# Optimization experiments

Hardware: AMD Instinct MI355X
Metric: run time of the kernel (lower is better)

The kernel has to match this reference:

```python
import jax, jax.numpy as jnp
import numpy as np

IMG_SIZE = 512
NUM_FREQ_MASKS = 4


def _make_masks(n, num):
    # Mirrors DCTTransform._generate_freq_masks: for i in reversed(range(num-1)),
    # an anti-triangular (low-frequency) mask of size n//2**i padded to (n,n),
    # then an all-ones mask appended last.
    masks = []
    for i in reversed(range(num - 1)):
        m = n // (2 ** i)
        tri = np.triu(np.ones((m, m), dtype=np.float32))      # upper triangular
        rot = np.rot90(tri, k=1)                               # -> i+j <= m-1 region
        pad = np.zeros((n, n), dtype=np.float32)
        pad[:m, :m] = rot
        masks.append(pad)
    masks.append(np.ones((n, n), dtype=np.float32))
    return np.stack(masks)  # [num, n, n]


def _dct_matrix(n, dtype=jnp.float32):
    # Orthonormal DCT-II matrix: X = D @ x  ==  scipy.fftpack.dct(x, axis=0, norm='ortho')
    k = jnp.arange(n, dtype=dtype)[:, None]
    m = jnp.arange(n, dtype=dtype)[None, :]
    D = jnp.cos(jnp.pi * (2.0 * m + 1.0) * k / (2.0 * n)) * jnp.sqrt(2.0 / n)
    D = D.at[0].multiply(1.0 / jnp.sqrt(2.0))  # k=0 row scale -> sqrt(1/n)
    return D


def setup_inputs() -> dict:
    key = jax.random.key(0)
    x = jax.random.normal(key, (32, 3, IMG_SIZE, IMG_SIZE), dtype=jnp.float32)
    masks = jnp.asarray(_make_masks(IMG_SIZE, NUM_FREQ_MASKS))
    return {"x": x, "masks": masks}


def reference(x, masks):
    # x: [B, C, H, W] with H == W == img_size; masks: [4, H, W]
    n = x.shape[-1]
    D = _dct_matrix(n, x.dtype)
    # 2D orthonormal DCT-II over last two axes: D @ x @ D^T (separable, order-free)
    dct2 = jnp.einsum('ij,bcjk,lk->bcil', D, x, D)
    outs = []
    for i in range(masks.shape[0]):  # small fixed loop over 4 masks
        masked = dct2 * masks[i]
        # inverse 2D DCT (IDCT-II == DCT-III, orthonormal): D^T @ y @ D
        outs.append(jnp.einsum('ji,bcjk,kl->bcil', D, masked, D))
    LH, HL, HH, LL = outs  # idx 0->LH, 1->HL, 2->HH, 3(ones)->LL per original forward
    return (LL, LH, HL, HH)
```

## Files before the change

### kernel.cpp

```cpp
#include <hip/hip_runtime.h>
#include <hip/hip_bf16.h>
#include <stdint.h>

#define NIMG 96
#define N 512
#define IMG (N*N)
#define OUT_PLANE ((long long)NIMG * IMG)

typedef __attribute__((ext_vector_type(8))) _Float16 f16x8;
typedef __attribute__((ext_vector_type(4))) float f32x4;
typedef unsigned short u16;

__device__ inline u16 f2h(float v) {
    _Float16 h = (_Float16)v;
    return __builtin_bit_cast(u16, h);
}

__device__ inline void gload16(const void* g, void* l) {
    __builtin_amdgcn_global_load_lds(
        (const __attribute__((address_space(1))) void*)g,
        (__attribute__((address_space(3))) void*)l, 16, 0, 0);
}

__global__ void build_D(u16* __restrict__ Drm, u16* __restrict__ Dcm) {
    int idx = blockIdx.x * 256 + threadIdx.x;
    int k = idx >> 9, m = idx & 511;
    int r = ((2 * m + 1) * k) & 2047;
    float c = cospif((float)r * (1.0f / 1024.0f));
    float s = (k == 0) ? 0.04419417382415922f : 0.0625f;
    u16 h = f2h(c * s);
    Drm[k * 512 + m] = h;
    Dcm[m * 512 + k] = h;
}

__global__ __launch_bounds__(256) void conv_x(const float* __restrict__ x,
                                              u16* __restrict__ Xcm) {
    __shared__ float t[32][33];
    const long long base = (long long)blockIdx.z * IMG;
    const int r0 = blockIdx.y * 32, c0 = blockIdx.x * 32;
    const int tr = threadIdx.x >> 3;
    const int tc = (threadIdx.x & 7) * 4;
    float4 v = *(const float4*)&x[base + (long long)(r0 + tr) * N + c0 + tc];
    t[tr][tc + 0] = v.x; t[tr][tc + 1] = v.y;
    t[tr][tc + 2] = v.z; t[tr][tc + 3] = v.w;
    __syncthreads();
    ushort4 h;
    h.x = f2h(t[tc + 0][tr]); h.y = f2h(t[tc + 1][tr]);
    h.z = f2h(t[tc + 2][tr]); h.w = f2h(t[tc + 3][tr]);
    *(ushort4*)&Xcm[base + (long long)(c0 + tr) * N + r0 + tc] = h;
}

__global__ __launch_bounds__(256) void maskcopy(const u16* __restrict__ Y,
                                                u16* __restrict__ Z,
                                                int W, int lim) {
    long long idx = (long long)blockIdx.x * 256 + threadIdx.x;
    int wq = W >> 2;
    long long perimg = (long long)W * wq;
    int img = (int)(idx / perimg);
    long long rem = idx % perimg;
    int j = (int)(rem / wq);
    int i = (int)(rem % wq) * 4;
    ushort4 v = *(const ushort4*)&Y[(long long)img * IMG + (long long)j * N + i];
    if (i + 0 + j > lim) v.x = 0;
    if (i + 1 + j > lim) v.y = 0;
    if (i + 2 + j > lim) v.z = 0;
    if (i + 3 + j > lim) v.w = 0;
    *(ushort4*)&Z[(long long)img * W * W + (long long)j * W + i] = v;
}

template<int EPI>
__global__ __launch_bounds__(256) void gemm16(
    const u16* __restrict__ A, long long sA, int lda,
    const u16* __restrict__ B, long long sB, int ldb,
    void* __restrict__ Cv, long long sC, int ldc,
    int K, int trilim)
{
    __shared__ u16 As[2][128 * 32];
    __shared__ u16 Bs[2][128 * 32];

    const int bz = blockIdx.z;
    const int m0 = blockIdx.y * 128;
    const int n0 = blockIdx.x * 128;
    const int tid = threadIdx.x;
    const int wave = tid >> 6;
    const int lane = tid & 63;

    const u16* __restrict__ Ab = A + (long long)bz * sA;
    const u16* __restrict__ Bb = B + (long long)bz * sB;

    const int srow = lane >> 2;
    const int sc8  = (lane & 3) * 8;
    const int war  = wave * 32;

    const int fr  = lane & 15;
    const int kg8 = (lane >> 4) * 8;
    const int wr  = (wave >> 1) * 64;
    const int wc  = (wave & 1) * 64;

    int aoff[4], boff[4];
    #pragma unroll
    for (int i = 0; i < 4; ++i) {
        aoff[i] = (wr + i * 16 + fr) * 32 + kg8;
        boff[i] = (wc + i * 16 + fr) * 32 + kg8;
    }

    f32x4 acc[4][4];
    #pragma unroll
    for (int i = 0; i < 4; ++i)
        #pragma unroll
        for (int j = 0; j < 4; ++j)
            acc[i][j] = (f32x4){0.0f, 0.0f, 0.0f, 0.0f};

    auto stage = [&](int buf, int k0) {
        #pragma unroll
        for (int i = 0; i < 2; ++i) {
            int r = war + i * 16;
            gload16(Ab + (long long)(m0 + r + srow) * lda + k0 + sc8, &As[buf][r * 32]);
            gload16(Bb + (long long)(n0 + r + srow) * ldb + k0 + sc8, &Bs[buf][r * 32]);
        }
    };
    auto compute = [&](int buf) {
        f16x8 af[4], bf[4];
        #pragma unroll
        for (int i = 0; i < 4; ++i) af[i] = *(const f16x8*)&As[buf][aoff[i]];
        #pragma unroll
        for (int j = 0; j < 4; ++j) bf[j] = *(const f16x8*)&Bs[buf][boff[j]];
        #pragma unroll
        for (int i = 0; i < 4; ++i)
            #pragma unroll
            for (int j = 0; j < 4; ++j)
                acc[i][j] = __builtin_amdgcn_mfma_f32_16x16x32_f16(af[i], bf[j], acc[i][j], 0, 0, 0);
    };

    const int nb = K >> 5;
    stage(0, 0);
    __syncthreads();
    int cur = 0;
    for (int t = 0; t < nb - 1; ++t) {
        stage(cur ^ 1, (t + 1) * 32);
        compute(cur);
        __syncthreads();
        cur ^= 1;
    }
    compute(cur);

    const int rb = (lane >> 4) * 4;
    if (EPI == 0) {
        float* Cb = (float*)Cv + (long long)bz * sC;
        #pragma unroll
        for (int i = 0; i < 4; ++i)
            #pragma unroll
            for (int j = 0; j < 4; ++j) {
                int r = m0 + wr + i * 16 + rb;
                int c = n0 + wc + j * 16 + fr;
                #pragma unroll
                for (int g = 0; g < 4; ++g)
                    Cb[(long long)(r + g) * ldc + c] = acc[i][j][g];
            }
    } else if (EPI == 1) {
        u16* Cb = (u16*)Cv + (long long)bz * sC;
        #pragma unroll
        for (int i = 0; i < 4; ++i)
            #pragma unroll
            for (int j = 0; j < 4; ++j) {
                int r = m0 + wr + i * 16 + rb;
                int c = n0 + wc + j * 16 + fr;
                #pragma unroll
                for (int g = 0; g < 4; ++g)
                    Cb[(long long)(r + g) * ldc + c] = f2h(acc[i][j][g]);
            }
    } else {
        u16* Cb = (u16*)Cv + (long long)bz * sC;
        #pragma unroll
        for (int i = 0; i < 4; ++i)
            #pragma unroll
            for (int j = 0; j < 4; ++j) {
                int r = m0 + wr + i * 16 + rb;
                int c = n0 + wc + j * 16 + fr;
                ushort4 h;
                float v0 = ((r + 0) + c <= trilim) ? acc[i][j][0] : 0.0f;
                float v1 = ((r + 1) + c <= trilim) ? acc[i][j][1] : 0.0f;
                float v2 = ((r + 2) + c <= trilim) ? acc[i][j][2] : 0.0f;
                float v3 = ((r + 3) + c <= trilim) ? acc[i][j][3] : 0.0f;
                h.x = f2h(v0); h.y = f2h(v1); h.z = f2h(v2); h.w = f2h(v3);
                *(ushort4*)&Cb[(long long)c * ldc + r] = h;
            }
    }
}

extern "C" void kernel_launch(void* const* d_in, const int* in_sizes, int n_in,
                              void* d_out, int out_size, void* d_ws, size_t ws_size,
                              hipStream_t stream) {
    const float* x = (const float*)d_in[0];
    float* out = (float*)d_out;
    float* outLL = out + 0 * OUT_PLANE;
    float* outLH = out + 1 * OUT_PLANE;
    float* outHL = out + 2 * OUT_PLANE;
    float* outHH = out + 3 * OUT_PLANE;

    char* ws = (char*)d_ws;
    u16* Drm = (u16*)(ws);
    u16* Dcm = (u16*)(ws + 524288);
    u16* Xcm = (u16*)(ws + 1048576);
    u16* Ycm = Xcm;
    char* reg = ws + 51380224;
    u16* T1 = (u16*)reg;
    u16* U  = (u16*)reg;
    u16* U2 = (u16*)reg;
    u16* U3 = (u16*)reg;
    u16* Y2 = (u16*)(reg + 25165824);
    u16* Y3 = (u16*)(reg + 37748736);

    const long long S = IMG;
    const int BIG = 1 << 30;

    build_D<<<dim3(IMG / 256), 256, 0, stream>>>(Drm, Dcm);
    conv_x<<<dim3(16, 16, NIMG), 256, 0, stream>>>(x, Xcm);

    gemm16<1><<<dim3(4, 4, NIMG), 256, 0, stream>>>(
        Drm, 0, 512, Xcm, S, 512, T1, S, 512, 512, 0);
    gemm16<2><<<dim3(4, 4, NIMG), 256, 0, stream>>>(
        T1, S, 512, Drm, 0, 512, Ycm, S, 512, 512, 511);
    gemm16<2><<<dim3(4, 4, NIMG), 256, 0, stream>>>(
        Ycm, S, 512, Dcm, 0, 512, U, S, 512, 512, BIG);
    gemm16<0><<<dim3(4, 4, NIMG), 256, 0, stream>>>(
        U, S, 512, Dcm, 0, 512, outHH, S, 512, 512, 0);

    maskcopy<<<dim3(NIMG * 256 * 256 / 4 / 256), 256, 0, stream>>>(Ycm, Y2, 256, 255);
    maskcopy<<<dim3(NIMG * 128 * 128 / 4 / 256), 256, 0, stream>>>(Ycm, Y3, 128, 127);

    gemm16<2><<<dim3(4, 2, NIMG), 256, 0, stream>>>(
        Y2, 256 * 256, 256, Dcm, 0, 512, U2, 512 * 256, 256, 256, BIG);
    gemm16<0><<<dim3(4, 4, NIMG), 256, 0, stream>>>(
        U2, 512 * 256, 256, Dcm, 0, 512, outHL, S, 512, 256, 0);

    gemm16<2><<<dim3(4, 1, NIMG), 256, 0, stream>>>(
        Y3, 128 * 128, 128, Dcm, 0, 512, U3, 512 * 128, 128, 128, BIG);
    gemm16<0><<<dim3(4, 4, NIMG), 256, 0, stream>>>(
        U3, 512 * 128, 128, Dcm, 0, 512, outLH, S, 512, 128, 0);

    hipMemcpyAsync(outLL, x, (size_t)OUT_PLANE * sizeof(float),
                   hipMemcpyDeviceToDevice, stream);
}
```

Before: 364.0 us.

## Restructure DCT GEMMs: full-K LDS staging, fused inverse launches, triangular skipping

Replaces the double-buffered 128x128 GEMM with a 256x64 tile kernel that stages the whole B panel into swizzled LDS once and streams A fragments straight from global memory. The three first-stage inverse GEMMs are fused into one launch (invA) that shortens K for the triangular-masked inputs, and the two low-band second-stage GEMMs are fused into invB. Tiles lying fully outside the triangular mask exit early. The LL copy is folded into the transpose kernel, and scratch buffers are moved into the HH output region. This adds LDS pressure and uncoalesced A loads from global memory, and depends on the HH output being written last.

Measured after the change: 481.1 us. 1.32x slower.

```diff
diff --git a/kernel.cpp b/kernel.cpp
--- a/kernel.cpp
+++ b/kernel.cpp
@@ -11,15 +11,9 @@
 typedef __attribute__((ext_vector_type(4))) float f32x4;
 typedef unsigned short u16;
 
-__device__ inline u16 f2h(float v) {
+__device__ __forceinline__ u16 f2h(float v) {
     _Float16 h = (_Float16)v;
     return __builtin_bit_cast(u16, h);
-}
-
-__device__ inline void gload16(const void* g, void* l) {
-    __builtin_amdgcn_global_load_lds(
-        (const __attribute__((address_space(1))) void*)g,
-        (__attribute__((address_space(3))) void*)l, 16, 0, 0);
 }
 
 __global__ void build_D(u16* __restrict__ Drm, u16* __restrict__ Dcm) {
@@ -34,13 +28,15 @@
 }
 
 __global__ __launch_bounds__(256) void conv_x(const float* __restrict__ x,
-                                              u16* __restrict__ Xcm) {
+                                              u16* __restrict__ Xcm,
+                                              float* __restrict__ outLL) {
     __shared__ float t[32][33];
     const long long base = (long long)blockIdx.z * IMG;
     const int r0 = blockIdx.y * 32, c0 = blockIdx.x * 32;
     const int tr = threadIdx.x >> 3;
     const int tc = (threadIdx.x & 7) * 4;
     float4 v = *(const float4*)&x[base + (long long)(r0 + tr) * N + c0 + tc];
+    *(float4*)&outLL[base + (long long)(r0 + tr) * N + c0 + tc] = v;
     t[tr][tc + 0] = v.x; t[tr][tc + 1] = v.y;
     t[tr][tc + 2] = v.z; t[tr][tc + 3] = v.w;
     __syncthreads();
@@ -68,91 +64,111 @@
     *(ushort4*)&Z[(long long)img * W * W + (long long)j * W + i] = v;
 }
 
+#define WAVE_DECLS                                                          \
+    const int wave = threadIdx.x >> 6;                                      \
+    const int lane = threadIdx.x & 63;                                      \
+    const int fr   = lane & 15;                                             \
+    const int kg8  = (lane >> 4) << 3;                                      \
+    const int rb   = (lane >> 4) << 2;
+
+#define GEMM_STAGE(Bp, ldb, Keff, lds, PITCHB)                              \
+    {                                                                       \
+        const int cpr = (Keff) >> 3;                \
+        const int csh = 31 - __builtin_clz(cpr);                            \
+        const int total = cpr << 6;                                        \
+        for (int c = threadIdx.x; c < total; c += 256) {                    \
+            int n  = c >> csh;                                              \
+            int kb = (c & (cpr - 1)) << 4;                                  \
+            f16x8 v = *(const f16x8*)((Bp) + (long long)n * (ldb) + (kb >> 1)); \
+            *(f16x8*)((u16*)(lds) + ((n * (PITCHB) + (kb ^ ((n & 7) << 4))) >> 1)) = v; \
+        }                                                                   \
+        __syncthreads();                                                    \
+    }
+
+#define GEMM_MAIN(Ab, lda, Keff, lds, PITCHB)                               \
+    f32x4 acc[4][4];                                                        \
+    _Pragma("unroll")                                                       \
+    for (int i = 0; i < 4; ++i)                                             \
+        _Pragma("unroll")                                                   \
+        for (int j = 0; j < 4; ++j)                                         \
+            acc[i][j] = (f32x4){0.0f, 0.0f, 0.0f, 0.0f};                    \
+    {                                                                       \
+        const u16* Aw = (Ab) + (long long)(wave * 64 + fr) * (lda) + kg8;   \
+        const long long astep = (long long)16 * (lda);                      \
+        int bb[4], bx[4];                                                   \
+        _Pragma("unroll")                                                   \
+        for (int j = 0; j < 4; ++j) {                                       \
+            int n = j * 16 + fr;                                            \
+            bb[j] = n * (PITCHB);                                           \
+            bx[j] = (n & 7) << 4;                                           \
+        }                                                                   \
+        const int nb = (Keff) >> 5;                                         \
+        f16x8 A0[4], A1[4];                                                 \
+        _Pragma("unroll")                                                   \
+        for (int i = 0; i < 4; ++i) A0[i] = *(const f16x8*)(Aw + i * astep);\
+        _Pragma("unroll")                                                   \
+        for (int i = 0; i < 4; ++i) A1[i] = *(const f16x8*)(Aw + i * astep + 32); \
+        for (int t = 0; t < nb; t += 2) {                                   \
+            f16x8 bf[4];                                                    \
+            _Pragma("unroll")                                               \
+            for (int j = 0; j < 4; ++j) {                                   \
+                int ko = ((kg8 << 1) + (t << 6)) ^ bx[j];                   \
+                bf[j] = *(const f16x8*)((const u16*)(lds) + ((bb[j] + ko) >> 1)); \
+            }                                                               \
+            _Pragma("unroll")                                               \
+            for (int i = 0; i < 4; ++i)                                     \
+                _Pragma("unroll")                                           \
+                for (int j = 0; j < 4; ++j)                                 \
+                    acc[i][j] = __builtin_amdgcn_mfma_f32_16x16x32_f16(A0[i], bf[j], acc[i][j], 0, 0, 0); \
+            if (t + 2 < nb) {                                               \
+                _Pragma("unroll")                                           \
+                for (int i = 0; i < 4; ++i) A0[i] = *(const f16x8*)(Aw + i * astep + (t + 2) * 32); \
+            }                                                               \
+            _Pragma("unroll")                                               \
+            for (int j = 0; j < 4; ++j) {                                   \
+                int ko = ((kg8 << 1) + ((t + 1) << 6)) ^ bx[j];             \
+                bf[j] = *(const f16x8*)((const u16*)(lds) + ((bb[j] + ko) >> 1)); \
+            }                                                               \
+            _Pragma("unroll")                                               \
+            for (int i = 0; i < 4; ++i)                                     \
+                _Pragma("unroll")                                           \
+                for (int j = 0; j < 4; ++j)                                 \
+                    acc[i][j] = __builtin_amdgcn_mfma_f32_16x16x32_f16(A1[i], bf[j], acc[i][j], 0, 0, 0); \
+            if (t + 3 < nb) {                                               \
+                _Pragma("unroll")                                           \
+                for (int i = 0; i < 4; ++i) A1[i] = *(const f16x8*)(Aw + i * astep + (t + 3) * 32); \
+            }                                                               \
+        }                                                                   \
+    }
+
 template<int EPI>
-__global__ __launch_bounds__(256) void gemm16(
+__global__ __launch_bounds__(256) void gemmS(
     const u16* __restrict__ A, long long sA, int lda,
     const u16* __restrict__ B, long long sB, int ldb,
     void* __restrict__ Cv, long long sC, int ldc,
     int K, int trilim)
 {
-    __shared__ u16 As[2][128 * 32];
-    __shared__ u16 Bs[2][128 * 32];
-
+    __shared__ u16 lds[32768];
     const int bz = blockIdx.z;
-    const int m0 = blockIdx.y * 128;
-    const int n0 = blockIdx.x * 128;
-    const int tid = threadIdx.x;
-    const int wave = tid >> 6;
-    const int lane = tid & 63;
-
-    const u16* __restrict__ Ab = A + (long long)bz * sA;
-    const u16* __restrict__ Bb = B + (long long)bz * sB;
-
-    const int srow = lane >> 2;
-    const int sc8  = (lane & 3) * 8;
-    const int war  = wave * 32;
-
-    const int fr  = lane & 15;
-    const int kg8 = (lane >> 4) * 8;
-    const int wr  = (wave >> 1) * 64;
-    const int wc  = (wave & 1) * 64;
-
-    int aoff[4], boff[4];
-    #pragma unroll
-    for (int i = 0; i < 4; ++i) {
-        aoff[i] = (wr + i * 16 + fr) * 32 + kg8;
-        boff[i] = (wc + i * 16 + fr) * 32 + kg8;
-    }
-
-    f32x4 acc[4][4];
-    #pragma unroll
-    for (int i = 0; i < 4; ++i)
-        #pragma unroll
-        for (int j = 0; j < 4; ++j)
-            acc[i][j] = (f32x4){0.0f, 0.0f, 0.0f, 0.0f};
-
-    auto stage = [&](int buf, int k0) {
-        #pragma unroll
-        for (int i = 0; i < 2; ++i) {
-            int r = war + i * 16;
-            gload16(Ab + (long long)(m0 + r + srow) * lda + k0 + sc8, &As[buf][r * 32]);
-            gload16(Bb + (long long)(n0 + r + srow) * ldb + k0 + sc8, &Bs[buf][r * 32]);
-        }
-    };
-    auto compute = [&](int buf) {
-        f16x8 af[4], bf[4];
-        #pragma unroll
-        for (int i = 0; i < 4; ++i) af[i] = *(const f16x8*)&As[buf][aoff[i]];
-        #pragma unroll
-        for (int j = 0; j < 4; ++j) bf[j] = *(const f16x8*)&Bs[buf][boff[j]];
-        #pragma unroll
-        for (int i = 0; i < 4; ++i)
-            #pragma unroll
-            for (int j = 0; j < 4; ++j)
-                acc[i][j] = __builtin_amdgcn_mfma_f32_16x16x32_f16(af[i], bf[j], acc[i][j], 0, 0, 0);
-    };
-
-    const int nb = K >> 5;
-    stage(0, 0);
-    __syncthreads();
-    int cur = 0;
-    for (int t = 0; t < nb - 1; ++t) {
-        stage(cur ^ 1, (t + 1) * 32);
-        compute(cur);
-        __syncthreads();
-        cur ^= 1;
-    }
-    compute(cur);
-
-    const int rb = (lane >> 4) * 4;
+    const int m0 = blockIdx.y * 256;
+    const int n0 = blockIdx.x * 64;
+    if (EPI == 2 && m0 + n0 > trilim) return;
+
+    WAVE_DECLS
+    const u16* Ab = A + (long long)bz * sA + (long long)m0 * lda;
+    const u16* Bp = B + (long long)bz * sB + (long long)n0 * ldb;
+
+    GEMM_STAGE(Bp, ldb, K, lds, 1024)
+    GEMM_MAIN(Ab, lda, K, lds, 1024)
+
     if (EPI == 0) {
         float* Cb = (float*)Cv + (long long)bz * sC;
         #pragma unroll
         for (int i = 0; i < 4; ++i)
             #pragma unroll
             for (int j = 0; j < 4; ++j) {
-                int r = m0 + wr + i * 16 + rb;
-                int c = n0 + wc + j * 16 + fr;
+                int r = m0 + wave * 64 + i * 16 + rb;
+                int c = n0 + j * 16 + fr;
                 #pragma unroll
                 for (int g = 0; g < 4; ++g)
                     Cb[(long long)(r + g) * ldc + c] = acc[i][j][g];
@@ -163,8 +179,8 @@
         for (int i = 0; i < 4; ++i)
             #pragma unroll
             for (int j = 0; j < 4; ++j) {
-                int r = m0 + wr + i * 16 + rb;
-                int c = n0 + wc + j * 16 + fr;
+                int r = m0 + wave * 64 + i * 16 + rb;
+                int c = n0 + j * 16 + fr;
                 #pragma unroll
                 for (int g = 0; g < 4; ++g)
                     Cb[(long long)(r + g) * ldc + c] = f2h(acc[i][j][g]);
@@ -175,17 +191,123 @@
         for (int i = 0; i < 4; ++i)
             #pragma unroll
             for (int j = 0; j < 4; ++j) {
-                int r = m0 + wr + i * 16 + rb;
-                int c = n0 + wc + j * 16 + fr;
+                int r = m0 + wave * 64 + i * 16 + rb;
+                int c = n0 + j * 16 + fr;
                 ushort4 h;
-                float v0 = ((r + 0) + c <= trilim) ? acc[i][j][0] : 0.0f;
-                float v1 = ((r + 1) + c <= trilim) ? acc[i][j][1] : 0.0f;
-                float v2 = ((r + 2) + c <= trilim) ? acc[i][j][2] : 0.0f;
-                float v3 = ((r + 3) + c <= trilim) ? acc[i][j][3] : 0.0f;
-                h.x = f2h(v0); h.y = f2h(v1); h.z = f2h(v2); h.w = f2h(v3);
+                h.x = f2h(((r + 0) + c <= trilim) ? acc[i][j][0] : 0.0f);
+                h.y = f2h(((r + 1) + c <= trilim) ? acc[i][j][1] : 0.0f);
+                h.z = f2h(((r + 2) + c <= trilim) ? acc[i][j][2] : 0.0f);
+                h.w = f2h(((r + 3) + c <= trilim) ? acc[i][j][3] : 0.0f);
                 *(ushort4*)&Cb[(long long)c * ldc + r] = h;
             }
     }
+}
+
+__global__ __launch_bounds__(256) void invA(
+    const u16* __restrict__ Ycm, const u16* __restrict__ Y2,
+    const u16* __restrict__ Y3, const u16* __restrict__ Dcm,
+    u16* __restrict__ U, u16* __restrict__ U2, u16* __restrict__ U3)
+{
+    __shared__ u16 lds[32768];
+    const int bz = blockIdx.z;
+    const int id = blockIdx.x;
+
+    const u16 *Ab, *Bp;
+    u16* Cb;
+    int lda, ldb, ldc, Keff, m0, n0;
+    bool cm;
+    if (id < 16) {
+        m0 = (id >> 3) * 256; n0 = (id & 7) * 64;
+        Ab = Ycm + (long long)bz * IMG + (long long)m0 * 512; lda = 512;
+        Bp = Dcm + (long long)n0 * 512;                        ldb = 512;
+        Cb = U + (long long)bz * IMG;                          ldc = 512;
+        Keff = 512 - m0; cm = true;
+    } else if (id < 24) {
+        int t2 = id - 16;
+        m0 = 0; n0 = t2 * 64;
+        Ab = Y2 + (long long)bz * 65536;                       lda = 256;
+        Bp = Dcm + (long long)n0 * 512;                        ldb = 512;
+        Cb = U2 + (long long)bz * 131072;                      ldc = 256;
+        Keff = 256; cm = true;
+    } else {
+        int t2 = id - 24;
+        m0 = (t2 >> 1) * 256; n0 = (t2 & 1) * 64;
+        Ab = Dcm + (long long)m0 * 512;                        lda = 512;
+        Bp = Y3 + (long long)bz * 16384 + (long long)n0 * 128; ldb = 128;
+        Cb = U3 + (long long)bz * 65536;                       ldc = 128;
+        Keff = 128; cm = false;
+    }
+
+    WAVE_DECLS
+    GEMM_STAGE(Bp, ldb, Keff, lds, 1024)
+    GEMM_MAIN(Ab, lda, Keff, lds, 1024)
+
+    if (cm) {
+        #pragma unroll
+        for (int i = 0; i < 4; ++i)
+            #pragma unroll
+            for (int j = 0; j < 4; ++j) {
+                int r = m0 + wave * 64 + i * 16 + rb;
+                int c = n0 + j * 16 + fr;
+                ushort4 h;
+                h.x = f2h(acc[i][j][0]); h.y = f2h(acc[i][j][1]);
+                h.z = f2h(acc[i][j][2]); h.w = f2h(acc[i][j][3]);
+                *(ushort4*)&Cb[(long long)c * ldc + r] = h;
+            }
+    } else {
+        #pragma unroll
+        for (int i = 0; i < 4; ++i)
+            #pragma unroll
+            for (int j = 0; j < 4; ++j) {
+                int r = m0 + wave * 64 + i * 16 + rb;
+                int c = n0 + j * 16 + fr;
+                #pragma unroll
+                for (int g = 0; g < 4; ++g)
+                    Cb[(long long)(r + g) * ldc + c] = f2h(acc[i][j][g]);
+            }
+    }
+}
+
+__global__ __launch_bounds__(256) void invB(
+    const u16* __restrict__ U2, const u16* __restrict__ U3,
+    const u16* __restrict__ Dcm,
+    float* __restrict__ outHL, float* __restrict__ outLH)
+{
+    __shared__ u16 lds[16384];
+    const int bz = blockIdx.z;
+    const int id = blockIdx.x;
+
+    const u16 *Ab, *Bp;
+    float* Cb;
+    int lda, Keff, m0, n0;
+    if (id < 16) {
+        m0 = (id >> 3) * 256; n0 = (id & 7) * 64;
+        Ab = U2 + (long long)bz * 131072 + (long long)m0 * 256; lda = 256;
+        Keff = 256;
+        Cb = outHL + (long long)bz * IMG;
+    } else {
+        int t2 = id - 16;
+        m0 = (t2 >> 3) * 256; n0 = (t2 & 7) * 64;
+        Ab = U3 + (long long)bz * 65536 + (long long)m0 * 128;  lda = 128;
+        Keff = 128;
+        Cb = outLH + (long long)bz * IMG;
+    }
+    Bp = Dcm + (long long)n0 * 512;
+
+    WAVE_DECLS
+    GEMM_STAGE(Bp, 512, Keff, lds, 512)
+    GEMM_MAIN(Ab, lda, Keff, lds, 512)
+
+    #pragma unroll
+    for (int i = 0; i < 4; ++i)
+        #pragma unroll
+        for (int j = 0; j < 4; ++j) {
+            int r = m0 + wave * 64 + i * 16 + rb;
+            int c = n0 + j * 16 + fr;
+            #pragma unroll
+            for (int g = 0; g < 4; ++g)
+                Cb[(long long)(r + g) * 512 + c] = acc[i][j][g];
+        }
 }
 
 extern "C" void kernel_launch(void* const* d_in, const int* in_sizes, int n_in,
@@ -206,39 +328,28 @@
     char* reg = ws + 51380224;
     u16* T1 = (u16*)reg;
     u16* U  = (u16*)reg;
-    u16* U2 = (u16*)reg;
-    u16* U3 = (u16*)reg;
-    u16* Y2 = (u16*)(reg + 25165824);
-    u16* Y3 = (u16*)(reg + 37748736);
+
+    u16* Y2 = (u16*)outHH;
+    u16* Y3 = Y2 + 6291456;
+    u16* U2 = Y3 + 1572864;
+    u16* U3 = U2 + 12582912;
 
     const long long S = IMG;
     const int BIG = 1 << 30;
 
     build_D<<<dim3(IMG / 256), 256, 0, stream>>>(Drm, Dcm);
-    conv_x<<<dim3(16, 16, NIMG), 256, 0, stream>>>(x, Xcm);
-
-    gemm16<1><<<dim3(4, 4, NIMG), 256, 0, stream>>>(
-        Drm, 0, 512, Xcm, S, 512, T1, S, 512, 512, 0);
-    gemm16<2><<<dim3(4, 4, NIMG), 256, 0, stream>>>(
+    conv_x<<<dim3(16, 16, NIMG), 256, 0, stream>>>(x, Xcm, outLL);
+
+    gemmS<1><<<dim3(8, 2, NIMG), 256, 0, stream>>>(
+        Drm, 0, 512, Xcm, S, 512, T1, S, 512, 512, BIG);
+    gemmS<2><<<dim3(8, 2, NIMG), 256, 0, stream>>>(
         T1, S, 512, Drm, 0, 512, Ycm, S, 512, 512, 511);
-    gemm16<2><<<dim3(4, 4, NIMG), 256, 0, stream>>>(
-        Ycm, S, 512, Dcm, 0, 512, U, S, 512, 512, BIG);
-    gemm16<0><<<dim3(4, 4, NIMG), 256, 0, stream>>>(
-        U, S, 512, Dcm, 0, 512, outHH, S, 512, 512, 0);
 
     maskcopy<<<dim3(NIMG * 256 * 256 / 4 / 256), 256, 0, stream>>>(Ycm, Y2, 256, 255);
     maskcopy<<<dim3(NIMG * 128 * 128 / 4 / 256), 256, 0, stream>>>(Ycm, Y3, 128, 127);
 
-    gemm16<2><<<dim3(4, 2, NIMG), 256, 0, stream>>>(
-        Y2, 256 * 256, 256, Dcm, 0, 512, U2, 512 * 256, 256, 256, BIG);
-    gemm16<0><<<dim3(4, 4, NIMG), 256, 0, stream>>>(
-        U2, 512 * 256, 256, Dcm, 0, 512, outHL, S, 512, 256, 0);
-
-    gemm16<2><<<dim3(4, 1, NIMG), 256, 0, stream>>>(
-        Y3, 128 * 128, 128, Dcm, 0, 512, U3, 512 * 128, 128, 128, BIG);
-    gemm16<0><<<dim3(4, 4, NIMG), 256, 0, stream>>>(
-        U3, 512 * 128, 128, Dcm, 0, 512, outLH, S, 512, 128, 0);
-
-    hipMemcpyAsync(outLL, x, (size_t)OUT_PLANE * sizeof(float),
-                   hipMemcpyDeviceToDevice, stream);
-}
+    invA<<<dim3(28, 1, NIMG), 256, 0, stream>>>(Ycm, Y2, Y3, Dcm, U, U2, U3);
+    invB<<<dim3(32, 1, NIMG), 256, 0, stream>>>(U2, U3, Dcm, outHL, outLH);
+    gemmS<0><<<dim3(8, 2, NIMG), 256, 0, stream>>>(
+        U, S, 512, Dcm, 0, 512, outHH, S, 512, 512, BIG);
+}
```
